# Optimization experiments

Hardware: AMD Instinct MI355X
Metric: run time of the kernel (lower is better)

Reference implementation:

```python
import jax, jax.numpy as jnp
import numpy as np

D = 1024

def setup_inputs() -> dict:
    key = jax.random.key(0)
    ks = jax.random.split(key, 12)
    B, N, d = 4, 4096, D
    init_std = 0.02 / np.sqrt(d)  # matches _init_weights for value_proj / o_proj
    inp = {
        "h": jax.random.normal(ks[0], (B, N, d), dtype=jnp.float32),
        # relation_encoder: Linear(d, d//2) -> GELU -> Linear(d//2, 1)  (weights stored [in, out])
        "W_re1": jax.random.normal(ks[1], (d, d // 2), dtype=jnp.float32) * 0.02,
        "b_re1": jnp.zeros((d // 2,), dtype=jnp.float32),
        "W_re2": jax.random.normal(ks[2], (d // 2, 1), dtype=jnp.float32) * 0.02,
        "b_re2": jnp.zeros((1,), dtype=jnp.float32),
        # value_proj: Linear(d, d, bias=False), init std = 0.02/sqrt(d)
        "W_v": jax.random.normal(ks[3], (d, d), dtype=jnp.float32) * init_std,
        # relation_transform: Linear(2d, d) -> GELU -> Linear(d, d)
        "W_rt1": jax.random.normal(ks[4], (2 * d, d), dtype=jnp.float32) * 0.02,
        "b_rt1": jnp.zeros((d,), dtype=jnp.float32),
        "W_rt2": jax.random.normal(ks[5], (d, d), dtype=jnp.float32) * 0.02,
        "b_rt2": jnp.zeros((d,), dtype=jnp.float32),
        # o_proj: Linear(d, d, bias=False), init std = 0.02/sqrt(d)
        "W_o": jax.random.normal(ks[6], (d, d), dtype=jnp.float32) * init_std,
    }
    return inp


def reference(h, W_re1, b_re1, W_re2, b_re2, W_v, W_rt1, b_rt1, W_rt2, b_rt2, W_o):
    B, N, d = h.shape
    # relation_encoder MLP -> scalar logit per token (torch GELU is exact erf form)
    hidden = jax.nn.gelu(jnp.einsum('bnd,dk->bnk', h, W_re1) + b_re1, approximate=False)
    relation_logits = (jnp.einsum('bnk,ko->bno', hidden, W_re2) + b_re2)[..., 0]  # [B, N]
    relation_strength = jax.nn.sigmoid(relation_logits)  # [B, N]
    # pointer targets: round(sigmoid * (N-1)) clamped (jnp.round == torch.round, half-to-even)
    relation_targets = jnp.clip(
        jnp.round(relation_strength * (N - 1)).astype(jnp.int32), 0, N - 1
    )  # [B, N]
    # per-token gather of target hidden state within each batch row
    target_features = jnp.take_along_axis(h, relation_targets[..., None], axis=1)  # [B, N, d]
    source_values = jnp.einsum('bnd,de->bne', h, W_v)
    target_values = jnp.einsum('bnd,de->bne', target_features, W_v)
    relation_input = jnp.concatenate([source_values, target_values], axis=-1)  # [B, N, 2d]
    relation_output = jax.nn.gelu(
        jnp.einsum('bnf,fe->bne', relation_input, W_rt1) + b_rt1, approximate=False
    )
    relation_output = jnp.einsum('bne,ef->bnf', relation_output, W_rt2) + b_rt2
    z = jnp.einsum('bnd,de->bne', relation_output, W_o)  # [B, N, d]
    return (z, relation_targets, relation_strength)
```

## Files before the change

### kernel.cpp

```cpp
#include <hip/hip_runtime.h>
#include <math.h>
#include <type_traits>

#define DMODEL 1024
#define NSEQ   4096
#define MTOT   16384

typedef unsigned short ushortT;
typedef __attribute__((ext_vector_type(8))) short short8;
typedef __attribute__((ext_vector_type(4))) float f32x4;

__device__ __forceinline__ float gelu_f(float x) {
    return 0.5f * x * (1.0f + erff(x * 0.70710678118654752440f));
}
__device__ __forceinline__ double gelu_d(double x) {
    return 0.5 * x * (1.0 + erf(x * 0.70710678118654752440));
}
__device__ __forceinline__ ushortT f2bf(float f) {
    unsigned u = __float_as_uint(f);
    u += 0x7FFFu + ((u >> 16) & 1u);
    return (ushortT)(u >> 16);
}
__device__ __forceinline__ float bf2f(ushortT b) {
    return __uint_as_float(((unsigned)b) << 16);
}
__device__ __forceinline__ void gload16(const void* g, void* l) {
    __builtin_amdgcn_global_load_lds(
        (const __attribute__((address_space(1))) unsigned*)g,
        (__attribute__((address_space(3))) unsigned*)l, 16, 0, 0);
}

enum { EPI_BIAS_F32 = 2, EPI_TRANS_BF16 = 3, EPI_PQ = 5 };

__device__ __forceinline__ int swz_off(int row, int slot) {
    return row * 64 + (((slot ^ (row & 7)) & 7) << 3);
}

template<int EPI, int NXT>
__global__ __launch_bounds__(512, 2)
void pipe_gemm(const ushortT* __restrict__ A, const ushortT* __restrict__ Bt,
               const float* __restrict__ bias, void* __restrict__ Cv,
               void* __restrict__ Cv2, int K, int lda, int ldb, int ldc, int cpx)
{
    __shared__ ushortT smem[4 * 16384];
    const int tid  = threadIdx.x;
    const int lane = tid & 63;
    const int w    = tid >> 6;
    const int wr   = w >> 2;
    const int wc   = w & 3;
    const int flat = blockIdx.x + blockIdx.y * NXT;
    const int swz  = (flat & 7) * cpx + (flat >> 3);
    const int n0   = (swz & (NXT - 1)) * 256;
    const int m0   = (swz / NXT) * 256;

    const int srow  = tid >> 3;
    const int sscol = (((tid & 7) ^ (srow & 7)) & 7) << 3;

#define STG_A(buf, q, k0) gload16(A  + (size_t)(m0 + (q)*64 + srow) * lda + (k0) + sscol, \
                                  (char*)smem + (buf)*32768 + (q)*8192 + w*1024)
#define STG_B(buf, q, k0) gload16(Bt + (size_t)(n0 + (q)*64 + srow) * ldb + (k0) + sscol, \
                                  (char*)smem + 65536 + (buf)*32768 + (q)*8192 + w*1024)
#define BAR() asm volatile("s_barrier" ::: "memory")

    f32x4 acc[8][4];
    #pragma unroll
    for (int i = 0; i < 8; i++)
        #pragma unroll
        for (int j = 0; j < 4; j++) acc[i][j] = (f32x4){0.f, 0.f, 0.f, 0.f};

    const int NT = K >> 6;

    #pragma unroll
    for (int q = 0; q < 4; q++) { STG_A(0, q, 0); STG_B(0, q, 0); }

    const int mi = lane & 15;
    const int g4 = lane >> 4;

    for (int t = 0; t < NT; ++t) {
        const int c  = t & 1;
        const int nb = c ^ 1;
        const int kn = (t + 1) << 6;
        const bool hn = (t + 1 < NT);

        if (hn) {
            STG_A(nb, 0, kn); STG_A(nb, 1, kn);
            asm volatile("s_waitcnt vmcnt(2)" ::: "memory");
        } else {
            asm volatile("s_waitcnt vmcnt(0)" ::: "memory");
        }
        BAR();

        short8 bf[4][2];
        #pragma unroll
        for (int nf = 0; nf < 4; nf++)
            #pragma unroll
            for (int ks = 0; ks < 2; ks++)
                bf[nf][ks] = *(const short8*)&smem[32768 + c * 16384 +
                                swz_off(wc * 64 + nf * 16 + mi, ks * 4 + g4)];

        #pragma unroll
        for (int p = 0; p < 4; p++) {
            if (p > 0) {
                if (hn) {
                    if (p == 1) { STG_A(nb, 2, kn); STG_A(nb, 3, kn); }
                    if (p == 2) { STG_B(nb, 0, kn); STG_B(nb, 1, kn); }
                    if (p == 3) { STG_B(nb, 2, kn); STG_B(nb, 3, kn); }
                }
                BAR();
            }
            short8 af[2][2];
            #pragma unroll
            for (int ii = 0; ii < 2; ii++)
                #pragma unroll
                for (int ks = 0; ks < 2; ks++)
                    af[ii][ks] = *(const short8*)&smem[c * 16384 +
                                    swz_off(wr * 128 + (p * 2 + ii) * 16 + mi, ks * 4 + g4)];
            __builtin_amdgcn_s_setprio(1);
            #pragma unroll
            for (int ks = 0; ks < 2; ks++)
                #pragma unroll
                for (int ii = 0; ii < 2; ii++)
                    #pragma unroll
                    for (int nf = 0; nf < 4; nf++)
                        acc[p * 2 + ii][nf] = __builtin_amdgcn_mfma_f32_16x16x32_bf16(
                            af[ii][ks], bf[nf][ks], acc[p * 2 + ii][nf], 0, 0, 0);
            __builtin_amdgcn_s_setprio(0);
        }
        BAR();
    }

    const int cr = (lane >> 4) * 4;
    #pragma unroll
    for (int i = 0; i < 8; i++) {
        #pragma unroll
        for (int j = 0; j < 4; j++) {
            const int gr = m0 + wr * 128 + i * 16 + cr;
            const int gc = n0 + wc * 64 + j * 16 + mi;
            #pragma unroll
            for (int r = 0; r < 4; r++) {
                float v = acc[i][j][r];
                if constexpr (EPI == EPI_BIAS_F32) {
                    ((float*)Cv)[(size_t)(gr + r) * ldc + gc] = v + bias[gc];
                } else {
                    if (gc < 1024)
                        ((float*)Cv)[(size_t)(gr + r) * ldc + gc] = v + bias[gc];
                    else
                        ((ushortT*)Cv2)[(size_t)(gr + r) * ldc + (gc - 1024)] = f2bf(v);
                }
            }
        }
    }
#undef STG_A
#undef STG_B
#undef BAR
}

template<int EPI, int NXT>
__global__ __launch_bounds__(256)
void mfma_gemm(const ushortT* __restrict__ A, const ushortT* __restrict__ Bt,
               const float* __restrict__ bias, void* __restrict__ Cv,
               void* __restrict__ Cv2, int K, int lda, int ldb, int ldc, int cpx)
{
    __shared__ ushortT As[128 * 32];
    __shared__ ushortT Bs[128 * 32];
    const int tid  = threadIdx.x;
    const int lane = tid & 63;
    const int w    = tid >> 6;
    const int wr   = (w >> 1) * 64;
    const int wc   = (w & 1) * 64;
    const int flat = blockIdx.x + blockIdx.y * NXT;
    const int swz  = (flat & 7) * cpx + (flat >> 3);
    const int n0   = (swz & (NXT - 1)) * 128;
    const int m0   = (swz / NXT) * 128;

    const int lrow = lane >> 2;
    const int lk   = (lane & 3) * 8;

    f32x4 acc[4][4];
    #pragma unroll
    for (int i = 0; i < 4; i++)
        #pragma unroll
        for (int j = 0; j < 4; j++) acc[i][j] = (f32x4){0.f, 0.f, 0.f, 0.f};

    for (int kk = 0; kk < K; kk += 32) {
        #pragma unroll
        for (int i = 0; i < 2; i++) {
            const ushortT* ga = A + (size_t)(m0 + w * 32 + i * 16 + lrow) * lda + kk + lk;
            gload16(ga, &As[(w * 32 + i * 16) * 32]);
            const ushortT* gb = Bt + (size_t)(n0 + w * 32 + i * 16 + lrow) * ldb + kk + lk;
            gload16(gb, &Bs[(w * 32 + i * 16) * 32]);
        }
        __syncthreads();

        const int mi = lane & 15;
        const int ko = (lane >> 4) * 8;
        short8 a[4], b[4];
        #pragma unroll
        for (int i = 0; i < 4; i++)
            a[i] = *(const short8*)&As[(wr + i * 16 + mi) * 32 + ko];
        #pragma unroll
        for (int j = 0; j < 4; j++)
            b[j] = *(const short8*)&Bs[(wc + j * 16 + mi) * 32 + ko];
        #pragma unroll
        for (int i = 0; i < 4; i++)
            #pragma unroll
            for (int j = 0; j < 4; j++)
                acc[i][j] = __builtin_amdgcn_mfma_f32_16x16x32_bf16(a[i], b[j], acc[i][j], 0, 0, 0);
        __syncthreads();
    }

    const int cr = (lane >> 4) * 4;
    const int cc = lane & 15;
    #pragma unroll
    for (int i = 0; i < 4; i++) {
        #pragma unroll
        for (int j = 0; j < 4; j++) {
            const int gr = m0 + wr + i * 16 + cr;
            const int gc = n0 + wc + j * 16 + cc;
            #pragma unroll
            for (int r = 0; r < 4; r++) {
                float v = acc[i][j][r];
                if constexpr (EPI == EPI_BIAS_F32)
                    ((float*)Cv)[(size_t)(gr + r) * ldc + gc] = v + bias[gc];
                else
                    ((ushortT*)Cv)[(size_t)gc * ldc + (gr + r)] = f2bf(v);
            }
        }
    }
}

__global__ __launch_bounds__(256)
void gelu_gather_k(const float* __restrict__ P, const ushortT* __restrict__ Q,
                   const int* __restrict__ gidx, ushortT* __restrict__ G)
{
    const int m = blockIdx.x;
    int t = gidx[m];
    t = max(0, min(t, MTOT - 1));
    const int c = threadIdx.x * 4;
    float4 p = *(const float4*)(P + (size_t)m * DMODEL + c);
    ushort4 q = *(const ushort4*)(Q + (size_t)t * DMODEL + c);
    ushortT o[4];
    o[0] = f2bf(gelu_f(p.x + bf2f(q.x)));
    o[1] = f2bf(gelu_f(p.y + bf2f(q.y)));
    o[2] = f2bf(gelu_f(p.z + bf2f(q.z)));
    o[3] = f2bf(gelu_f(p.w + bf2f(q.w)));
    *(ulong1*)(G + (size_t)m * DMODEL + c) = *(ulong1*)o;
}

__global__ __launch_bounds__(256)
void wsplit_gemm(const ushortT* __restrict__ Ah, const ushortT* __restrict__ Al,
                 const ushortT* __restrict__ Bh0, const ushortT* __restrict__ Bl0,
                 ushortT* __restrict__ Ct0, int K, int lda, int ldb, int ldc)
{
    __shared__ ushortT Ash[128 * 32], Asl[128 * 32];
    __shared__ ushortT Bsh[128 * 32], Bsl[128 * 32];
    const int tid  = threadIdx.x;
    const int lane = tid & 63;
    const int w    = tid >> 6;
    const int wr   = (w >> 1) * 64;
    const int wc   = (w & 1) * 64;
    const int sel  = blockIdx.y >> 3;
    const int m0   = (blockIdx.y & 7) * 128;
    const int n0   = blockIdx.x * 128;
    const ushortT* Bh = Bh0 + sel * 1024;
    const ushortT* Bl = Bl0 + sel * 1024;
    ushortT* Ct = Ct0 + (size_t)sel * 1024 * 1024;
    const int lrow = lane >> 2;
    const int lk   = (lane & 3) * 8;

    f32x4 acc[4][4];
    #pragma unroll
    for (int i = 0; i < 4; i++)
        #pragma unroll
        for (int j = 0; j < 4; j++) acc[i][j] = (f32x4){0.f, 0.f, 0.f, 0.f};

    for (int kk = 0; kk < K; kk += 32) {
        #pragma unroll
        for (int i = 0; i < 2; i++) {
            const size_t aoff = (size_t)(m0 + w * 32 + i * 16 + lrow) * lda + kk + lk;
            const size_t boff = (size_t)(n0 + w * 32 + i * 16 + lrow) * ldb + kk + lk;
            const int ldst = (w * 32 + i * 16) * 32;
            gload16(Ah + aoff, &Ash[ldst]);
            gload16(Al + aoff, &Asl[ldst]);
            gload16(Bh + boff, &Bsh[ldst]);
            gload16(Bl + boff, &Bsl[ldst]);
        }
        __syncthreads();

        const int mi = lane & 15;
        const int ko = (lane >> 4) * 8;
        short8 ah[4], al[4], bh[4], bl[4];
        #pragma unroll
        for (int i = 0; i < 4; i++) {
            ah[i] = *(const short8*)&Ash[(wr + i * 16 + mi) * 32 + ko];
            al[i] = *(const short8*)&Asl[(wr + i * 16 + mi) * 32 + ko];
        }
        #pragma unroll
        for (int j = 0; j < 4; j++) {
            bh[j] = *(const short8*)&Bsh[(wc + j * 16 + mi) * 32 + ko];
            bl[j] = *(const short8*)&Bsl[(wc + j * 16 + mi) * 32 + ko];
        }
        #pragma unroll
        for (int i = 0; i < 4; i++)
            #pragma unroll
            for (int j = 0; j < 4; j++) {
                acc[i][j] = __builtin_amdgcn_mfma_f32_16x16x32_bf16(ah[i], bh[j], acc[i][j], 0, 0, 0);
                acc[i][j] = __builtin_amdgcn_mfma_f32_16x16x32_bf16(ah[i], bl[j], acc[i][j], 0, 0, 0);
                acc[i][j] = __builtin_amdgcn_mfma_f32_16x16x32_bf16(al[i], bh[j], acc[i][j], 0, 0, 0);
            }
        __syncthreads();
    }

    const int cr = (lane >> 4) * 4;
    const int cc = lane & 15;
    #pragma unroll
    for (int i = 0; i < 4; i++)
        #pragma unroll
        for (int j = 0; j < 4; j++) {
            const int gr = m0 + wr + i * 16 + cr;
            const int gc = n0 + wc + j * 16 + cc;
            #pragma unroll
            for (int r = 0; r < 4; r++)
                Ct[(size_t)gc * ldc + (gr + r)] = f2bf(acc[i][j][r]);
        }
}

__global__ __launch_bounds__(256)
void enc_gemm(const ushortT* __restrict__ Ah, const ushortT* __restrict__ Al,
              const ushortT* __restrict__ Bh, const ushortT* __restrict__ Bl,
              const float* __restrict__ bias, float* __restrict__ C)
{
    __shared__ ushortT Ash[128 * 32], Asl[128 * 32];
    __shared__ ushortT Bsh[128 * 32], Bsl[128 * 32];
    const int tid  = threadIdx.x;
    const int lane = tid & 63;
    const int w    = tid >> 6;
    const int wr   = (w >> 1) * 64;
    const int wc   = (w & 1) * 64;
    const int flat = blockIdx.x + (blockIdx.y << 2);
    const int swz  = (flat & 7) * 64 + (flat >> 3);
    const int n0   = (swz & 3) * 128;
    const int m0   = (swz >> 2) * 128;
    const int lrow = lane >> 2;
    const int lk   = (lane & 3) * 8;

    f32x4 acc[4][4];
    #pragma unroll
    for (int i = 0; i < 4; i++)
        #pragma unroll
        for (int j = 0; j < 4; j++) acc[i][j] = (f32x4){0.f, 0.f, 0.f, 0.f};

    for (int kk = 0; kk < DMODEL; kk += 32) {
        #pragma unroll
        for (int i = 0; i < 2; i++) {
            const size_t aoff = (size_t)(m0 + w * 32 + i * 16 + lrow) * DMODEL + kk + lk;
            const size_t boff = (size_t)(n0 + w * 32 + i * 16 + lrow) * DMODEL + kk + lk;
            const int ldst = (w * 32 + i * 16) * 32;
            gload16(Ah + aoff, &Ash[ldst]);
            gload16(Al + aoff, &Asl[ldst]);
            gload16(Bh + boff, &Bsh[ldst]);
            gload16(Bl + boff, &Bsl[ldst]);
        }
        __syncthreads();

        const int mi = lane & 15;
        const int ko = (lane >> 4) * 8;
        short8 ah[4], al[4], bh[4], bl[4];
        #pragma unroll
        for (int i = 0; i < 4; i++) {
            ah[i] = *(const short8*)&Ash[(wr + i * 16 + mi) * 32 + ko];
            al[i] = *(const short8*)&Asl[(wr + i * 16 + mi) * 32 + ko];
        }
        #pragma unroll
        for (int j = 0; j < 4; j++) {
            bh[j] = *(const short8*)&Bsh[(wc + j * 16 + mi) * 32 + ko];
            bl[j] = *(const short8*)&Bsl[(wc + j * 16 + mi) * 32 + ko];
        }
        #pragma unroll
        for (int i = 0; i < 4; i++)
            #pragma unroll
            for (int j = 0; j < 4; j++) {
                acc[i][j] = __builtin_amdgcn_mfma_f32_16x16x32_bf16(ah[i], bh[j], acc[i][j], 0, 0, 0);
                acc[i][j] = __builtin_amdgcn_mfma_f32_16x16x32_bf16(ah[i], bl[j], acc[i][j], 0, 0, 0);
                acc[i][j] = __builtin_amdgcn_mfma_f32_16x16x32_bf16(al[i], bh[j], acc[i][j], 0, 0, 0);
            }
        __syncthreads();
    }

    const int cr = (lane >> 4) * 4;
    const int cc = lane & 15;
    #pragma unroll
    for (int i = 0; i < 4; i++)
        #pragma unroll
        for (int j = 0; j < 4; j++) {
            const int gr = m0 + wr + i * 16 + cr;
            const int gc = n0 + wc + j * 16 + cc;
            #pragma unroll
            for (int r = 0; r < 4; r++)
                C[(size_t)(gr + r) * 512 + gc] = gelu_f(acc[i][j][r] + bias[gc]);
        }
}

__global__ __launch_bounds__(256)
void target2_k(const float* __restrict__ Genc, const float* __restrict__ W2,
               const float* __restrict__ b2, float* __restrict__ outT,
               float* __restrict__ outS, int* __restrict__ gidx,
               int* __restrict__ cnt, int* __restrict__ list)
{
    const int m = blockIdx.x * 4 + (threadIdx.x >> 6);
    const int lane = threadIdx.x & 63;
    const float* gr = Genc + (size_t)m * 512;
    double s = 0.0;
    #pragma unroll 4
    for (int j = lane; j < 512; j += 64) s = fma((double)gr[j], (double)W2[j], s);
    #pragma unroll
    for (int off = 32; off; off >>= 1) s += __shfl_down(s, off);
    if (lane == 0) {
        double logit = s + (double)b2[0];
        double str = 1.0 / (1.0 + exp(-logit));
        double r = str * (double)(NSEQ - 1);
        double n = rint(r);
        double dist = fabs(r - n);
        n = fmin(fmax(n, 0.0), (double)(NSEQ - 1));
        int t = (int)n;
        outT[m] = (float)t;
        outS[m] = (float)str;
        gidx[m] = ((m >> 12) << 12) + t;
        if (dist > 0.46) {
            int ix = atomicAdd(cnt, 1) & (MTOT - 1);
            list[ix] = m;
        }
    }
}

#define FIX_T 4
__global__ __launch_bounds__(1024)
void fixup_k(const float* __restrict__ h, const float* __restrict__ W1,
             const float* __restrict__ b1, const float* __restrict__ W2,
             const float* __restrict__ b2, const int* __restrict__ cnt_p,
             const int* __restrict__ list, float* __restrict__ outT,
             float* __restrict__ outS, int* __restrict__ gidx)
{
    __shared__ float  hrow[FIX_T][1024];
    __shared__ double part[FIX_T][4][512];
    __shared__ double red[FIX_T][8];
    const int tid = threadIdx.x;
    const int kg  = tid >> 8;
    const int jj  = tid & 255;
    const int cnt = min(*cnt_p, MTOT);
    for (int base = (int)blockIdx.x * FIX_T; base < cnt;
         base += (int)gridDim.x * FIX_T) {
        const int nt = min(FIX_T, cnt - base);
        for (int t = 0; t < nt; t++) {
            const int m = list[base + t];
            hrow[t][tid] = h[(size_t)m * 1024 + tid];
        }
        __syncthreads();

        double a0[FIX_T], a1[FIX_T];
        #pragma unroll
        for (int t = 0; t < FIX_T; t++) { a0[t] = 0.0; a1[t] = 0.0; }
        const int kbase = kg * 256;
        #pragma unroll 4
        for (int kk = 0; kk < 256; kk++) {
            const int k = kbase + kk;
            const double wa = (double)W1[(size_t)k * 512 + jj];
            const double wb = (double)W1[(size_t)k * 512 + jj + 256];
            #pragma unroll
            for (int t = 0; t < FIX_T; t++) {
                const double hv = (double)hrow[t][k];
                a0[t] = fma(hv, wa, a0[t]);
                a1[t] = fma(hv, wb, a1[t]);
            }
        }
        #pragma unroll
        for (int t = 0; t < FIX_T; t++) {
            part[t][kg][jj]       = a0[t];
            part[t][kg][jj + 256] = a1[t];
        }
        __syncthreads();

        if (tid < 512) {
            const int col  = tid;
            const int lane = tid & 63;
            const int wv   = tid >> 6;
            const double b1c = (double)b1[col];
            const double w2c = (double)W2[col];
            #pragma unroll
            for (int t = 0; t < FIX_T; t++) {
                double hid = part[t][0][col] + part[t][1][col]
                           + part[t][2][col] + part[t][3][col] + b1c;
                double v = gelu_d(hid) * w2c;
                #pragma unroll
                for (int off = 32; off; off >>= 1) v += __shfl_down(v, off);
                if (lane == 0) red[t][wv] = v;
            }
        }
        __syncthreads();
        if (tid < nt) {
            const int t = tid;
            double logit = (double)b2[0];
            #pragma unroll
            for (int q = 0; q < 8; q++) logit += red[t][q];
            double str = 1.0 / (1.0 + exp(-logit));
            double r = str * (double)(NSEQ - 1);
            double n = rint(r);
            n = fmin(fmax(n, 0.0), (double)(NSEQ - 1));
            const int m = list[base + t];
            const int ti = (int)n;
            outT[m] = (float)ti;
            outS[m] = (float)str;
            gidx[m] = ((m >> 12) << 12) + ti;
        }
        __syncthreads();
    }
}

__global__ __launch_bounds__(256)
void biascomb_k(const float* __restrict__ brt2, const float* __restrict__ Wo,
                float* __restrict__ bc)
{
    int j = blockIdx.x * 256 + threadIdx.x;
    float s = 0.f;
    for (int e = 0; e < DMODEL; e++) s = fmaf(brt2[e], Wo[e * DMODEL + j], s);
    bc[j] = s;
}

__global__ __launch_bounds__(256)
void cast_k(const float* __restrict__ x, ushortT* __restrict__ y, int n)
{
    int i = (blockIdx.x * 256 + threadIdx.x) * 4;
    if (i < n) {
        float4 v = *(const float4*)(x + i);
        ushortT o[4] = { f2bf(v.x), f2bf(v.y), f2bf(v.z), f2bf(v.w) };
        *(ulong1*)&y[i] = *(ulong1*)o;
    }
}

__global__ __launch_bounds__(256)
void split_cast_k(const float* __restrict__ x, ushortT* __restrict__ yh,
                  ushortT* __restrict__ yl, int n)
{
    int i = (blockIdx.x * 256 + threadIdx.x) * 4;
    if (i < n) {
        float4 v = *(const float4*)(x + i);
        float vv[4] = { v.x, v.y, v.z, v.w };
        ushortT oh[4], ol[4];
        #pragma unroll
        for (int q = 0; q < 4; q++) {
            oh[q] = f2bf(vv[q]);
            ol[q] = f2bf(vv[q] - bf2f(oh[q]));
        }
        *(ulong1*)&yh[i] = *(ulong1*)oh;
        *(ulong1*)&yl[i] = *(ulong1*)ol;
    }
}

__global__ __launch_bounds__(256)
void transcast_k(const float* __restrict__ W, ushortT* __restrict__ Wt, int K, int N)
{
    __shared__ float t[32][33];
    const int tx = threadIdx.x & 31, ty = threadIdx.x >> 5;
    const int n0 = blockIdx.x * 32, k0 = blockIdx.y * 32;
    #pragma unroll
    for (int r = 0; r < 32; r += 8)
        t[ty + r][tx] = W[(size_t)(k0 + ty + r) * N + n0 + tx];
    __syncthreads();
    #pragma unroll
    for (int r = 0; r < 32; r += 8)
        Wt[(size_t)(n0 + ty + r) * K + k0 + tx] = f2bf(t[tx][ty + r]);
}

__global__ __launch_bounds__(256)
void split_transcast_k(const float* __restrict__ W, ushortT* __restrict__ Wth,
                       ushortT* __restrict__ Wtl, int K, int N)
{
    __shared__ float t[32][33];
    const int tx = threadIdx.x & 31, ty = threadIdx.x >> 5;
    const int n0 = blockIdx.x * 32, k0 = blockIdx.y * 32;
    #pragma unroll
    for (int r = 0; r < 32; r += 8)
        t[ty + r][tx] = W[(size_t)(k0 + ty + r) * N + n0 + tx];
    __syncthreads();
    #pragma unroll
    for (int r = 0; r < 32; r += 8) {
        float x = t[tx][ty + r];
        ushortT hi = f2bf(x);
        Wth[(size_t)(n0 + ty + r) * K + k0 + tx] = hi;
        Wtl[(size_t)(n0 + ty + r) * K + k0 + tx] = f2bf(x - bf2f(hi));
    }
}

extern "C" void kernel_launch(void* const* d_in, const int* in_sizes, int n_in,
                              void* d_out, int out_size, void* d_ws, size_t ws_size,
                              hipStream_t stream)
{
    const float* h     = (const float*)d_in[0];
    const float* W_re1 = (const float*)d_in[1];
    const float* b_re1 = (const float*)d_in[2];
    const float* W_re2 = (const float*)d_in[3];
    const float* b_re2 = (const float*)d_in[4];
    const float* W_v   = (const float*)d_in[5];
    const float* W_rt1 = (const float*)d_in[6];
    const float* b_rt1 = (const float*)d_in[7];
    const float* W_rt2 = (const float*)d_in[8];
    const float* b_rt2 = (const float*)d_in[9];
    const float* W_o   = (const float*)d_in[10];

    float* z    = (float*)d_out;
    float* outT = z + (size_t)MTOT * DMODEL;
    float* outS = outT + MTOT;
    ushortT* Q    = (ushortT*)z;
    ushortT* h_hi = (ushortT*)z + (size_t)MTOT * DMODEL;

    char* ws = (char*)d_ws;
    ushortT* G       = (ushortT*)ws;
    float*   Genc    = (float*)(ws + (32ull  << 20));
    ushortT* h_lo    = (ushortT*)(ws + (64ull  << 20));
    float*   P       = (float*)(ws + (32ull  << 20));
    ushortT* Wrt1t_h = (ushortT*)(ws + (96ull  << 20));
    ushortT* Wrt1t_l = (ushortT*)(ws + (100ull << 20));
    ushortT* Wv_h    = (ushortT*)(ws + (104ull << 20));
    ushortT* Wv_l    = (ushortT*)(ws + (106ull << 20));
    ushortT* Wa_t    = (ushortT*)(ws + (108ull << 20));
    ushortT* Wo_t    = (ushortT*)(ws + (112ull << 20));
    ushortT* Wrt2_b  = (ushortT*)(ws + (114ull << 20));
    ushortT* Wc_t    = (ushortT*)(ws + (116ull << 20));
    ushortT* Wre1t_h = (ushortT*)(ws + (118ull << 20));
    ushortT* Wre1t_l = (ushortT*)(ws + (119ull << 20));
    float*   b_c     = (float*)(ws + (120ull << 20));
    int*     cnt     = (int*)  (ws + (120ull << 20) + 4096);
    int*     gidx    = (int*)  (ws + (120ull << 20) + 8192);
    int*     list    = (int*)  (ws + (120ull << 20) + 8192 + 65536);

    split_cast_k<<<dim3(MTOT * DMODEL / 1024), 256, 0, stream>>>(h, h_hi, h_lo, MTOT * DMODEL);
    split_cast_k<<<dim3(DMODEL * DMODEL / 1024), 256, 0, stream>>>(W_v, Wv_h, Wv_l, DMODEL * DMODEL);
    split_transcast_k<<<dim3(16, 32), 256, 0, stream>>>(W_re1, Wre1t_h, Wre1t_l, DMODEL, 512);
    split_transcast_k<<<dim3(32, 64), 256, 0, stream>>>(W_rt1, Wrt1t_h, Wrt1t_l, 2 * DMODEL, DMODEL);
    cast_k<<<dim3(DMODEL * DMODEL / 1024), 256, 0, stream>>>(W_rt2, Wrt2_b, DMODEL * DMODEL);
    transcast_k<<<dim3(32, 32), 256, 0, stream>>>(W_o, Wo_t, DMODEL, DMODEL);
    biascomb_k<<<dim3(4), 256, 0, stream>>>(b_rt2, W_o, b_c);

    wsplit_gemm<<<dim3(8, 16), 256, 0, stream>>>(Wv_h, Wv_l, Wrt1t_h, Wrt1t_l,
                                                 Wa_t, DMODEL, DMODEL, 2 * DMODEL, DMODEL);

    enc_gemm<<<dim3(4, 128), 256, 0, stream>>>(h_hi, h_lo, Wre1t_h, Wre1t_l, b_re1, Genc);

    hipMemsetAsync(cnt, 0, 4, stream);
    target2_k<<<dim3(MTOT / 4), 256, 0, stream>>>(Genc, W_re2, b_re2, outT, outS, gidx, cnt, list);
    fixup_k<<<dim3(1024), 1024, 0, stream>>>(h, W_re1, b_re1, W_re2, b_re2, cnt, list,
                                             outT, outS, gidx);

    mfma_gemm<EPI_TRANS_BF16, 8><<<dim3(8, 8), 256, 0, stream>>>(
        Wrt2_b, Wo_t, nullptr, (void*)Wc_t, nullptr, DMODEL, DMODEL, DMODEL, DMODEL, 8);

    pipe_gemm<EPI_PQ, 8><<<dim3(8, 64), 512, 0, stream>>>(
        h_hi, Wa_t, b_rt1, (void*)P, (void*)Q, DMODEL, DMODEL, DMODEL, DMODEL, 64);

    gelu_gather_k<<<dim3(MTOT), 256, 0, stream>>>(P, Q, gidx, G);

    pipe_gemm<EPI_BIAS_F32, 4><<<dim3(4, 64), 512, 0, stream>>>(
        G, Wc_t, b_c, (void*)z, nullptr, DMODEL, DMODEL, DMODEL, DMODEL, 32);
}
```

Measured before the change: 584.0 us.

## Run encoder split-bf16 GEMM through pipelined kernel as K-concatenated 3-pass GEMM

Replaces the dedicated 128x128 encoder GEMM, which did hi/lo split products, with the 256x256 pipelined GEMM. The three split products are expressed as one GEMM over K=3072 that picks hi/lo A and B pointers per K range, and GELU is applied in a new epilogue. It also simplifies the pipelined GEMM's staging: all loads for the next tile are issued at once after a full vmcnt(0) wait and a single barrier, instead of being interleaved across the compute phases with partial waits. This affects the other two GEMMs as well and may reduce load/compute overlap there. The encoder grid becomes only 128 blocks, which may underfill the GPU.

```diff
diff --git a/kernel.cpp b/kernel.cpp
--- a/kernel.cpp
+++ b/kernel.cpp
@@ -30,15 +30,16 @@
         (__attribute__((address_space(3))) unsigned*)l, 16, 0, 0);
 }
 
-enum { EPI_BIAS_F32 = 2, EPI_TRANS_BF16 = 3, EPI_PQ = 5 };
+enum { EPI_BIAS_F32 = 2, EPI_TRANS_BF16 = 3, EPI_PQ = 5, EPI_GELU_ENC = 6 };
 
 __device__ __forceinline__ int swz_off(int row, int slot) {
     return row * 64 + (((slot ^ (row & 7)) & 7) << 3);
 }
 
-template<int EPI, int NXT>
+template<int EPI, int NXT, bool SPLIT3>
 __global__ __launch_bounds__(512, 2)
-void pipe_gemm(const ushortT* __restrict__ A, const ushortT* __restrict__ Bt,
+void pipe_gemm(const ushortT* __restrict__ A, const ushortT* __restrict__ A2,
+               const ushortT* __restrict__ Bt, const ushortT* __restrict__ B2,
                const float* __restrict__ bias, void* __restrict__ Cv,
                void* __restrict__ Cv2, int K, int lda, int ldb, int ldc, int cpx)
 {
@@ -56,11 +57,24 @@
     const int srow  = tid >> 3;
     const int sscol = (((tid & 7) ^ (srow & 7)) & 7) << 3;
 
-#define STG_A(buf, q, k0) gload16(A  + (size_t)(m0 + (q)*64 + srow) * lda + (k0) + sscol, \
-                                  (char*)smem + (buf)*32768 + (q)*8192 + w*1024)
-#define STG_B(buf, q, k0) gload16(Bt + (size_t)(n0 + (q)*64 + srow) * ldb + (k0) + sscol, \
-                                  (char*)smem + 65536 + (buf)*32768 + (q)*8192 + w*1024)
-#define BAR() asm volatile("s_barrier" ::: "memory")
+    auto stage = [&](int buf, int kt) {
+        const ushortT* Ab; const ushortT* Bb; int kl;
+        if constexpr (SPLIT3) {
+            const int kn = kt << 6;
+            Ab = (kn >= 2048) ? A2 : A;
+            Bb = (kn >= 1024 && kn < 2048) ? B2 : Bt;
+            kl = kn & 1023;
+        } else {
+            Ab = A; Bb = Bt; kl = kt << 6;
+        }
+        #pragma unroll
+        for (int q = 0; q < 4; q++) {
+            gload16(Ab + (size_t)(m0 + q * 64 + srow) * lda + kl + sscol,
+                    (char*)smem + buf * 32768 + q * 8192 + w * 1024);
+            gload16(Bb + (size_t)(n0 + q * 64 + srow) * ldb + kl + sscol,
+                    (char*)smem + 65536 + buf * 32768 + q * 8192 + w * 1024);
+        }
+    };
 
     f32x4 acc[8][4];
     #pragma unroll
@@ -70,25 +84,16 @@
 
     const int NT = K >> 6;
 
-    #pragma unroll
-    for (int q = 0; q < 4; q++) { STG_A(0, q, 0); STG_B(0, q, 0); }
+    stage(0, 0);
 
     const int mi = lane & 15;
     const int g4 = lane >> 4;
 
     for (int t = 0; t < NT; ++t) {
-        const int c  = t & 1;
-        const int nb = c ^ 1;
-        const int kn = (t + 1) << 6;
-        const bool hn = (t + 1 < NT);
-
-        if (hn) {
-            STG_A(nb, 0, kn); STG_A(nb, 1, kn);
-            asm volatile("s_waitcnt vmcnt(2)" ::: "memory");
-        } else {
-            asm volatile("s_waitcnt vmcnt(0)" ::: "memory");
-        }
-        BAR();
+        const int c = t & 1;
+        asm volatile("s_waitcnt vmcnt(0)" ::: "memory");
+        asm volatile("s_barrier" ::: "memory");
+        if (t + 1 < NT) stage(c ^ 1, t + 1);
 
         short8 bf[4][2];
         #pragma unroll
@@ -100,14 +105,6 @@
 
         #pragma unroll
         for (int p = 0; p < 4; p++) {
-            if (p > 0) {
-                if (hn) {
-                    if (p == 1) { STG_A(nb, 2, kn); STG_A(nb, 3, kn); }
-                    if (p == 2) { STG_B(nb, 0, kn); STG_B(nb, 1, kn); }
-                    if (p == 3) { STG_B(nb, 2, kn); STG_B(nb, 3, kn); }
-                }
-                BAR();
-            }
             short8 af[2][2];
             #pragma unroll
             for (int ii = 0; ii < 2; ii++)
@@ -126,7 +123,6 @@
                             af[ii][ks], bf[nf][ks], acc[p * 2 + ii][nf], 0, 0, 0);
             __builtin_amdgcn_s_setprio(0);
         }
-        BAR();
     }
 
     const int cr = (lane >> 4) * 4;
@@ -141,6 +137,8 @@
                 float v = acc[i][j][r];
                 if constexpr (EPI == EPI_BIAS_F32) {
                     ((float*)Cv)[(size_t)(gr + r) * ldc + gc] = v + bias[gc];
+                } else if constexpr (EPI == EPI_GELU_ENC) {
+                    ((float*)Cv)[(size_t)(gr + r) * ldc + gc] = gelu_f(v + bias[gc]);
                 } else {
                     if (gc < 1024)
                         ((float*)Cv)[(size_t)(gr + r) * ldc + gc] = v + bias[gc];
@@ -150,9 +148,6 @@
             }
         }
     }
-#undef STG_A
-#undef STG_B
-#undef BAR
 }
 
 template<int EPI, int NXT>
@@ -322,82 +317,6 @@
             #pragma unroll
             for (int r = 0; r < 4; r++)
                 Ct[(size_t)gc * ldc + (gr + r)] = f2bf(acc[i][j][r]);
-        }
-}
-
-__global__ __launch_bounds__(256)
-void enc_gemm(const ushortT* __restrict__ Ah, const ushortT* __restrict__ Al,
-              const ushortT* __restrict__ Bh, const ushortT* __restrict__ Bl,
-              const float* __restrict__ bias, float* __restrict__ C)
-{
-    __shared__ ushortT Ash[128 * 32], Asl[128 * 32];
-    __shared__ ushortT Bsh[128 * 32], Bsl[128 * 32];
-    const int tid  = threadIdx.x;
-    const int lane = tid & 63;
-    const int w    = tid >> 6;
-    const int wr   = (w >> 1) * 64;
-    const int wc   = (w & 1) * 64;
-    const int flat = blockIdx.x + (blockIdx.y << 2);
-    const int swz  = (flat & 7) * 64 + (flat >> 3);
-    const int n0   = (swz & 3) * 128;
-    const int m0   = (swz >> 2) * 128;
-    const int lrow = lane >> 2;
-    const int lk   = (lane & 3) * 8;
-
-    f32x4 acc[4][4];
-    #pragma unroll
-    for (int i = 0; i < 4; i++)
-        #pragma unroll
-        for (int j = 0; j < 4; j++) acc[i][j] = (f32x4){0.f, 0.f, 0.f, 0.f};
-
-    for (int kk = 0; kk < DMODEL; kk += 32) {
-        #pragma unroll
-        for (int i = 0; i < 2; i++) {
-            const size_t aoff = (size_t)(m0 + w * 32 + i * 16 + lrow) * DMODEL + kk + lk;
-            const size_t boff = (size_t)(n0 + w * 32 + i * 16 + lrow) * DMODEL + kk + lk;
-            const int ldst = (w * 32 + i * 16) * 32;
-            gload16(Ah + aoff, &Ash[ldst]);
-            gload16(Al + aoff, &Asl[ldst]);
-            gload16(Bh + boff, &Bsh[ldst]);
-            gload16(Bl + boff, &Bsl[ldst]);
-        }
-        __syncthreads();
-
-        const int mi = lane & 15;
-        const int ko = (lane >> 4) * 8;
-        short8 ah[4], al[4], bh[4], bl[4];
-        #pragma unroll
-        for (int i = 0; i < 4; i++) {
-            ah[i] = *(const short8*)&Ash[(wr + i * 16 + mi) * 32 + ko];
-            al[i] = *(const short8*)&Asl[(wr + i * 16 + mi) * 32 + ko];
-        }
-        #pragma unroll
-        for (int j = 0; j < 4; j++) {
-            bh[j] = *(const short8*)&Bsh[(wc + j * 16 + mi) * 32 + ko];
-            bl[j] = *(const short8*)&Bsl[(wc + j * 16 + mi) * 32 + ko];
-        }
-        #pragma unroll
-        for (int i = 0; i < 4; i++)
-            #pragma unroll
-            for (int j = 0; j < 4; j++) {
-                acc[i][j] = __builtin_amdgcn_mfma_f32_16x16x32_bf16(ah[i], bh[j], acc[i][j], 0, 0, 0);
-                acc[i][j] = __builtin_amdgcn_mfma_f32_16x16x32_bf16(ah[i], bl[j], acc[i][j], 0, 0, 0);
-                acc[i][j] = __builtin_amdgcn_mfma_f32_16x16x32_bf16(al[i], bh[j], acc[i][j], 0, 0, 0);
-            }
-        __syncthreads();
-    }
-
-    const int cr = (lane >> 4) * 4;
-    const int cc = lane & 15;
-    #pragma unroll
-    for (int i = 0; i < 4; i++)
-        #pragma unroll
-        for (int j = 0; j < 4; j++) {
-            const int gr = m0 + wr + i * 16 + cr;
-            const int gc = n0 + wc + j * 16 + cc;
-            #pragma unroll
-            for (int r = 0; r < 4; r++)
-                C[(size_t)(gr + r) * 512 + gc] = gelu_f(acc[i][j][r] + bias[gc]);
         }
 }
 
@@ -644,7 +563,9 @@
     wsplit_gemm<<<dim3(8, 16), 256, 0, stream>>>(Wv_h, Wv_l, Wrt1t_h, Wrt1t_l,
                                                  Wa_t, DMODEL, DMODEL, 2 * DMODEL, DMODEL);
 
-    enc_gemm<<<dim3(4, 128), 256, 0, stream>>>(h_hi, h_lo, Wre1t_h, Wre1t_l, b_re1, Genc);
+    pipe_gemm<EPI_GELU_ENC, 2, true><<<dim3(2, 64), 512, 0, stream>>>(
+        h_hi, h_lo, Wre1t_h, Wre1t_l, b_re1, (void*)Genc, nullptr,
+        3 * DMODEL, DMODEL, DMODEL, 512, 16);
 
     hipMemsetAsync(cnt, 0, 4, stream);
     target2_k<<<dim3(MTOT / 4), 256, 0, stream>>>(Genc, W_re2, b_re2, outT, outS, gidx, cnt, list);
@@ -654,11 +575,13 @@
     mfma_gemm<EPI_TRANS_BF16, 8><<<dim3(8, 8), 256, 0, stream>>>(
         Wrt2_b, Wo_t, nullptr, (void*)Wc_t, nullptr, DMODEL, DMODEL, DMODEL, DMODEL, 8);
 
-    pipe_gemm<EPI_PQ, 8><<<dim3(8, 64), 512, 0, stream>>>(
-        h_hi, Wa_t, b_rt1, (void*)P, (void*)Q, DMODEL, DMODEL, DMODEL, DMODEL, 64);
+    pipe_gemm<EPI_PQ, 8, false><<<dim3(8, 64), 512, 0, stream>>>(
+        h_hi, nullptr, Wa_t, nullptr, b_rt1, (void*)P, (void*)Q,
+        DMODEL, DMODEL, DMODEL, DMODEL, 64);
 
     gelu_gather_k<<<dim3(MTOT), 256, 0, stream>>>(P, Q, gidx, G);
 
-    pipe_gemm<EPI_BIAS_F32, 4><<<dim3(4, 64), 512, 0, stream>>>(
-        G, Wc_t, b_c, (void*)z, nullptr, DMODEL, DMODEL, DMODEL, DMODEL, 32);
-}
+    pipe_gemm<EPI_BIAS_F32, 4, false><<<dim3(4, 64), 512, 0, stream>>>(
+        G, nullptr, Wc_t, nullptr, b_c, (void*)z, nullptr,
+        DMODEL, DMODEL, DMODEL, DMODEL, 32);
+}
```

Measured after the change: 619.4 us. 1.06x slower.
